# Optimization experiments

Measured on AMD Instinct MI355X. Metric: run time of the kernel, lower is better.

## Reference

```python
import jax, jax.numpy as jnp
import numpy as np

EMB = 8
HID = 64
B = 1000
T = 512
N = (B * T) // 5  # events per source; sources partition the (batch,time) grid

_KEYS = ["ccba", "cdtx", "cust", "dp", "remit"]
_NUMS = {"ccba": 8, "cdtx": 1, "cust": 1, "dp": 2, "remit": 1}
_CATS = {"ccba": 0, "cdtx": 2, "cust": 3, "dp": 8, "remit": 1}
_VOCAB = {"ccba": 0, "cdtx": 179, "cust": 37, "dp": 435, "remit": 5}


def setup_inputs() -> dict:
    ks = iter(jax.random.split(jax.random.key(0), 64))
    rng = np.random.default_rng(0)
    chunks = np.split(rng.permutation(B * T), 5)
    d = {}
    for k5, ch in zip(_KEYS, chunks):
        d[k5 + "_num"] = jax.random.normal(next(ks), (N, _NUMS[k5]), jnp.float32)
        if _CATS[k5] > 0:
            d[k5 + "_cat"] = jax.random.randint(next(ks), (N, _CATS[k5]), 0, _VOCAB[k5])
            d[k5 + "_tab"] = jax.random.normal(next(ks), (_VOCAB[k5], EMB), jnp.float32) * 0.1
        d[k5 + "_bi"] = jnp.asarray(ch // T, jnp.int32)
        d[k5 + "_ti"] = jnp.asarray(ch % T, jnp.int32)
        in_dim = _CATS[k5] * EMB + _NUMS[k5]
        d[k5 + "_W"] = jax.random.normal(next(ks), (in_dim, HID), jnp.float32) * np.float32(1.0 / np.sqrt(in_dim))
        d[k5 + "_b"] = jnp.zeros((HID,), jnp.float32)
    # LSTM: 2 layers x 2 directions, hidden 64, proj_size 1 -> layer1 input is 2
    for l, insz in [(0, HID), (1, 2)]:
        d[f"Wih{l}"] = jax.random.normal(next(ks), (2, 4 * HID, insz), jnp.float32) * 0.05
        d[f"Whh{l}"] = jax.random.normal(next(ks), (2, 4 * HID, 1), jnp.float32) * 0.05
        d[f"Whr{l}"] = jax.random.normal(next(ks), (2, 1, HID), jnp.float32) * 0.05
        d[f"bih{l}"] = jnp.zeros((2, 4 * HID), jnp.float32)
        d[f"bhh{l}"] = jnp.zeros((2, 4 * HID), jnp.float32)
    d["length"] = T
    d["batch_size"] = B
    return d


def _embed(num, cat, tab, W, b):
    # FeatureEmbedder: concat(categorical embeddings, numeric) -> Linear(hidden)
    x = num if cat is None else jnp.concatenate([tab[cat].reshape(cat.shape[0], -1), num], axis=-1)
    return x @ W + b


def _lstm_dir(x, Wih, Whh, Whr, bih, bhh, reverse):
    Bx = x.shape[0]
    H = Whr.shape[1]
    p = Whr.shape[0]
    bias = bih + bhh

    def step(carry, xt):
        h, c = carry  # h: [B,p] projected hidden, c: [B,H] cell
        g = xt @ Wih.T + h @ Whh.T + bias
        i, f, gg, o = jnp.split(g, 4, axis=-1)  # PyTorch gate order i,f,g,o
        c = jax.nn.sigmoid(f) * c + jax.nn.sigmoid(i) * jnp.tanh(gg)
        h = (jax.nn.sigmoid(o) * jnp.tanh(c)) @ Whr.T  # proj_size projection
        return (h, c), h

    init = (jnp.zeros((Bx, p), x.dtype), jnp.zeros((Bx, H), x.dtype))
    _, ys = jax.lax.scan(step, init, jnp.swapaxes(x, 0, 1), reverse=reverse)
    return jnp.swapaxes(ys, 0, 1)  # [B,T,p]


def _bilstm(x, Wih, Whh, Whr, bih, bhh):
    fwd = _lstm_dir(x, Wih[0], Whh[0], Whr[0], bih[0], bhh[0], False)
    bwd = _lstm_dir(x, Wih[1], Whh[1], Whr[1], bih[1], bhh[1], True)
    return jnp.concatenate([fwd, bwd], axis=-1)


def _forward(a):
    feat = jnp.zeros((a["batch_size"], a["length"], HID), jnp.float32)
    for k5 in _KEYS:
        v = _embed(a[k5 + "_num"], a.get(k5 + "_cat"), a.get(k5 + "_tab"), a[k5 + "_W"], a[k5 + "_b"])
        feat = feat.at[a[k5 + "_bi"], a[k5 + "_ti"]].set(v)  # scatter-assemble padded tensor
    h = _bilstm(feat, a["Wih0"], a["Whh0"], a["Whr0"], a["bih0"], a["bhh0"])
    h = _bilstm(h, a["Wih1"], a["Whh1"], a["Whr1"], a["bih1"], a["bhh1"])
    return h.mean(axis=2)  # [B,T]


def reference(ccba_num, ccba_bi, ccba_ti, ccba_W, ccba_b,
              cdtx_num, cdtx_cat, cdtx_tab, cdtx_bi, cdtx_ti, cdtx_W, cdtx_b,
              cust_num, cust_cat, cust_tab, cust_bi, cust_ti, cust_W, cust_b,
              dp_num, dp_cat, dp_tab, dp_bi, dp_ti, dp_W, dp_b,
              remit_num, remit_cat, remit_tab, remit_bi, remit_ti, remit_W, remit_b,
              Wih0, Whh0, Whr0, bih0, bhh0, Wih1, Whh1, Whr1, bih1, bhh1,
              length, batch_size):
    return _forward(dict(locals()))
```

## Files before the change

kernel.cpp:

```cpp
#include <hip/hip_runtime.h>
#include <cstdint>
#include <cstddef>

#define TLEN 512
#define BATCH 1000
#define NEVS 102400
#define HID 64
#define W0S 32

__device__ __forceinline__ float fast_rcp(float x) {
#if __has_builtin(__builtin_amdgcn_rcpf)
    return __builtin_amdgcn_rcpf(x);
#else
    return 1.0f / x;
#endif
}
__device__ __forceinline__ float sigm(float x) { return fast_rcp(1.0f + __expf(-x)); }
__device__ __forceinline__ float tanh_f(float x) { return fmaf(2.0f, sigm(2.0f * x), -1.0f); }

__device__ __forceinline__ float wave_sum_bcast(float x) {
#if __has_builtin(__builtin_amdgcn_update_dpp) && __has_builtin(__builtin_amdgcn_readlane)
    x += __int_as_float(__builtin_amdgcn_update_dpp(0, __float_as_int(x), 0x111, 0xf, 0xf, true));
    x += __int_as_float(__builtin_amdgcn_update_dpp(0, __float_as_int(x), 0x112, 0xf, 0xf, true));
    x += __int_as_float(__builtin_amdgcn_update_dpp(0, __float_as_int(x), 0x114, 0xf, 0xf, true));
    x += __int_as_float(__builtin_amdgcn_update_dpp(0, __float_as_int(x), 0x118, 0xf, 0xf, true));
    x += __int_as_float(__builtin_amdgcn_update_dpp(0, __float_as_int(x), 0x142, 0xa, 0xf, true));
    x += __int_as_float(__builtin_amdgcn_update_dpp(0, __float_as_int(x), 0x143, 0xc, 0xf, true));
    return __int_as_float(__builtin_amdgcn_readlane(__float_as_int(x), 63));
#else
#pragma unroll
    for (int off = 1; off < 64; off <<= 1) x += __shfl_xor(x, off, 64);
    return x;
#endif
}

__global__ __launch_bounds__(256) void map_build_kernel(
    const int* __restrict__ b0, const int* __restrict__ t0,
    const int* __restrict__ b1, const int* __restrict__ t1,
    const int* __restrict__ b2, const int* __restrict__ t2,
    const int* __restrict__ b3, const int* __restrict__ t3,
    const int* __restrict__ b4, const int* __restrict__ t4,
    int* __restrict__ map)
{
    const int src = blockIdx.y;
    const int* bi = src == 0 ? b0 : src == 1 ? b1 : src == 2 ? b2 : src == 3 ? b3 : b4;
    const int* ti = src == 0 ? t0 : src == 1 ? t1 : src == 2 ? t2 : src == 3 ? t3 : t4;
    const int e = blockIdx.x * 256 + threadIdx.x;
    map[bi[e] * TLEN + ti[e]] = (src << 20) | e;
}

__global__ __launch_bounds__(512) void compose_kernel(
    const float* __restrict__ W0, const float* __restrict__ B0,
    const float* __restrict__ W1, const float* __restrict__ B1,
    const float* __restrict__ W2, const float* __restrict__ B2,
    const float* __restrict__ W3, const float* __restrict__ B3,
    const float* __restrict__ W4, const float* __restrict__ B4,
    const float* __restrict__ Wih, const float* __restrict__ bih,
    const float* __restrict__ bhh, float* __restrict__ wp)
{
    const int col = threadIdx.x;
    const int row = blockIdx.x;
    const float* srcW; const float* srcB; int base, IND;
    if (row < 9)        { srcW = W0; srcB = B0; base = 0;   IND = 8;  }
    else if (row < 27)  { srcW = W1; srcB = B1; base = 9;   IND = 17; }
    else if (row < 53)  { srcW = W2; srcB = B2; base = 27;  IND = 25; }
    else if (row < 120) { srcW = W3; srcB = B3; base = 53;  IND = 66; }
    else                { srcW = W4; srcB = B4; base = 120; IND = 9;  }
    const int j = row - base;
    const float* xrow = (j < IND) ? (srcW + (size_t)j * 64) : srcB;
    const float* wr = Wih + (size_t)col * 64;
    float acc = 0.0f;
#pragma unroll
    for (int h2 = 0; h2 < 64; ++h2) acc = fmaf(xrow[h2], wr[h2], acc);
    if (j == IND) acc += bih[col] + bhh[col];
    wp[(size_t)row * 512 + col] = acc;
}

__global__ __launch_bounds__(256) void fused0_kernel(
    const float* __restrict__ ccba_num,
    const float* __restrict__ cdtx_num, const int* __restrict__ cdtx_cat, const float* __restrict__ cdtx_tab,
    const float* __restrict__ cust_num, const int* __restrict__ cust_cat, const float* __restrict__ cust_tab,
    const float* __restrict__ dp_num,   const int* __restrict__ dp_cat,   const float* __restrict__ dp_tab,
    const float* __restrict__ remit_num, const int* __restrict__ remit_cat, const float* __restrict__ remit_tab,
    const float* __restrict__ wp, const int* __restrict__ map,
    const float* __restrict__ Whh, const float* __restrict__ Whr,
    float* __restrict__ h0)
{
    const int tid = threadIdx.x;
    const int b = blockIdx.x >> 1, dir = blockIdx.x & 1;
    const int col = dir * 256 + tid;

    float w_c0[9], w_c1[18], w_c2[26], w_c3[67], w_c4[10];
#pragma unroll
    for (int j = 0; j < 9;  ++j) w_c0[j] = wp[(size_t)(0   + j) * 512 + col];
#pragma unroll
    for (int j = 0; j < 18; ++j) w_c1[j] = wp[(size_t)(9   + j) * 512 + col];
#pragma unroll
    for (int j = 0; j < 26; ++j) w_c2[j] = wp[(size_t)(27  + j) * 512 + col];
#pragma unroll
    for (int j = 0; j < 67; ++j) w_c3[j] = wp[(size_t)(53  + j) * 512 + col];
#pragma unroll
    for (int j = 0; j < 10; ++j) w_c4[j] = wp[(size_t)(120 + j) * 512 + col];

    __shared__ float window[W0S * 256];
    __shared__ float xbuf[W0S][68];
    __shared__ int   mcls[W0S];

    const int lane = tid & 63;
    float whh4[4] = {0, 0, 0, 0};
    float whr = 0.0f, h = 0.0f, c = 0.0f;
    if (tid < 64) {
#pragma unroll
        for (int k = 0; k < 4; ++k) whh4[k] = Whh[dir * 256 + k * 64 + lane];
        whr = Whr[dir * HID + lane];
    }
    float* h0p = h0 + (size_t)b * TLEN * 2 + dir;

    auto dot_evt = [&](int mc, const float* xb) -> float {
        const int src = mc >> 20;
        float a0 = 0.0f, a1 = 0.0f, bias = 0.0f;
        switch (src) {
        case 0:
#pragma unroll
            for (int j = 0; j < 8; j += 2) { a0 = fmaf(xb[j], w_c0[j], a0); a1 = fmaf(xb[j + 1], w_c0[j + 1], a1); }
            bias = w_c0[8]; break;
        case 1:
#pragma unroll
            for (int j = 0; j < 16; j += 2) { a0 = fmaf(xb[j], w_c1[j], a0); a1 = fmaf(xb[j + 1], w_c1[j + 1], a1); }
            a0 = fmaf(xb[16], w_c1[16], a0);
            bias = w_c1[17]; break;
        case 2:
#pragma unroll
            for (int j = 0; j < 24; j += 2) { a0 = fmaf(xb[j], w_c2[j], a0); a1 = fmaf(xb[j + 1], w_c2[j + 1], a1); }
            a0 = fmaf(xb[24], w_c2[24], a0);
            bias = w_c2[25]; break;
        case 3:
#pragma unroll
            for (int j = 0; j < 66; j += 2) { a0 = fmaf(xb[j], w_c3[j], a0); a1 = fmaf(xb[j + 1], w_c3[j + 1], a1); }
            bias = w_c3[66]; break;
        default:
#pragma unroll
            for (int j = 0; j < 8; j += 2) { a0 = fmaf(xb[j], w_c4[j], a0); a1 = fmaf(xb[j + 1], w_c4[j + 1], a1); }
            a0 = fmaf(xb[8], w_c4[8], a0);
            bias = w_c4[9]; break;
        }
        return bias + a0 + a1;
    };

    for (int s0 = 0; s0 < TLEN; s0 += W0S) {
        {
            const int sl = tid >> 3, q = tid & 7;
            const int s = s0 + sl;
            const int t = dir ? (TLEN - 1 - s) : s;
            const int mc = map[b * TLEN + t];
            if (q == 0) mcls[sl] = mc;
            const int src = mc >> 20, e = mc & 0xFFFFF;
            switch (src) {
            case 0:
                for (int v = q; v < 8; v += 8) xbuf[sl][v] = ccba_num[(size_t)e * 8 + v];
                break;
            case 1:
                for (int v = q; v < 17; v += 8) {
                    float x = (v < 16) ? cdtx_tab[(size_t)cdtx_cat[e * 2 + (v >> 3)] * 8 + (v & 7)]
                                       : cdtx_num[e];
                    xbuf[sl][v] = x;
                }
                break;
            case 2:
                for (int v = q; v < 25; v += 8) {
                    float x = (v < 24) ? cust_tab[(size_t)cust_cat[e * 3 + (v >> 3)] * 8 + (v & 7)]
                                       : cust_num[e];
                    xbuf[sl][v] = x;
                }
                break;
            case 3:
                for (int v = q; v < 66; v += 8) {
                    float x = (v < 64) ? dp_tab[(size_t)dp_cat[e * 8 + (v >> 3)] * 8 + (v & 7)]
                                       : dp_num[(size_t)e * 2 + (v - 64)];
                    xbuf[sl][v] = x;
                }
                break;
            default:
                for (int v = q; v < 9; v += 8) {
                    float x = (v < 8) ? remit_tab[(size_t)remit_cat[e] * 8 + v]
                                      : remit_num[e];
                    xbuf[sl][v] = x;
                }
                break;
            }
        }
        __syncthreads();

        for (int sl = 0; sl < W0S; sl += 2) {
            const float accA = dot_evt(mcls[sl], xbuf[sl]);
            const float accB = dot_evt(mcls[sl + 1], xbuf[sl + 1]);
            window[sl * 256 + tid] = accA;
            window[(sl + 1) * 256 + tid] = accB;
        }
        __syncthreads();

        if (tid < 64) {
            float G[4], N[4];
#pragma unroll
            for (int k = 0; k < 4; ++k) G[k] = window[k * 64 + lane];
            for (int sl = 0; sl < W0S; ++sl) {
                const int slp = (sl + 1 < W0S) ? (sl + 1) : sl;
#pragma unroll
                for (int k = 0; k < 4; ++k) N[k] = window[slp * 256 + k * 64 + lane];
                const float gi = fmaf(whh4[0], h, G[0]);
                const float gf = fmaf(whh4[1], h, G[1]);
                const float gg = fmaf(whh4[2], h, G[2]);
                const float go = fmaf(whh4[3], h, G[3]);
                c = sigm(gf) * c + sigm(gi) * tanh_f(gg);
                h = wave_sum_bcast(sigm(go) * tanh_f(c) * whr);
                const int s = s0 + sl;
                const int t = dir ? (TLEN - 1 - s) : s;
                if (lane == 0) h0p[(size_t)t * 2] = h;
#pragma unroll
                for (int k = 0; k < 4; ++k) G[k] = N[k];
            }
        }
        __syncthreads();
    }
}

__global__ __launch_bounds__(256) void lstm1_kernel(
    const float* __restrict__ h0, const float* __restrict__ Wih,
    const float* __restrict__ Whh, const float* __restrict__ Whr,
    const float* __restrict__ bih, const float* __restrict__ bhh,
    float* __restrict__ h1)
{
    int w = threadIdx.x >> 6, lane = threadIdx.x & 63;
    int p = blockIdx.x * 4 + w;
    int b = p >> 1, dir = p & 1;

    float wi0[4], wi1[4], whh[4], bias[4];
#pragma unroll
    for (int k = 0; k < 4; ++k) {
        int r = k * 64 + lane;
        wi0[k] = Wih[(size_t)(dir * 256 + r) * 2 + 0];
        wi1[k] = Wih[(size_t)(dir * 256 + r) * 2 + 1];
        whh[k] = Whh[dir * 256 + r];
        bias[k] = bih[dir * 256 + r] + bhh[dir * 256 + r];
    }
    float whr = Whr[dir * HID + lane];
    float h = 0.0f, c = 0.0f;
    const float* hb = h0 + (size_t)b * TLEN * 2;

    auto xat = [&](int t) -> float2 {
        int tc = t < TLEN ? t : TLEN - 1;
        int tt = dir ? (TLEN - 1 - tc) : tc;
        return *(const float2*)(hb + (size_t)tt * 2);
    };

    float2 xA = xat(0), xB = xat(1);
    for (int t = 0; t < TLEN; t += 2) {
        float2 xC = xat(t + 2), xD = xat(t + 3);
        {
            float g[4];
#pragma unroll
            for (int k = 0; k < 4; ++k)
                g[k] = fmaf(whh[k], h, fmaf(wi1[k], xA.y, fmaf(wi0[k], xA.x, bias[k])));
            c = sigm(g[1]) * c + sigm(g[0]) * tanh_f(g[2]);
            h = wave_sum_bcast(sigm(g[3]) * tanh_f(c) * whr);
            int tt = dir ? (TLEN - 1 - t) : t;
            if (lane == 0) h1[((size_t)b * TLEN + tt) * 2 + dir] = h;
        }
        {
            float g[4];
#pragma unroll
            for (int k = 0; k < 4; ++k)
                g[k] = fmaf(whh[k], h, fmaf(wi1[k], xB.y, fmaf(wi0[k], xB.x, bias[k])));
            c = sigm(g[1]) * c + sigm(g[0]) * tanh_f(g[2]);
            h = wave_sum_bcast(sigm(g[3]) * tanh_f(c) * whr);
            int tt = dir ? (TLEN - 2 - t) : (t + 1);
            if (lane == 0) h1[((size_t)b * TLEN + tt) * 2 + dir] = h;
        }
        xA = xC; xB = xD;
    }
}

__global__ __launch_bounds__(256) void mean_kernel(
    const float2* __restrict__ h1, float* __restrict__ out)
{
    int i = blockIdx.x * 256 + threadIdx.x;
    if (i < BATCH * TLEN) {
        float2 v = h1[i];
        out[i] = 0.5f * (v.x + v.y);
    }
}

extern "C" void kernel_launch(void* const* d_in, const int* in_sizes, int n_in,
                              void* d_out, int out_size, void* d_ws, size_t ws_size,
                              hipStream_t stream)
{
    const float* ccba_num = (const float*)d_in[0];
    const int*   ccba_bi  = (const int*)d_in[1];
    const int*   ccba_ti  = (const int*)d_in[2];
    const float* ccba_W   = (const float*)d_in[3];
    const float* ccba_b   = (const float*)d_in[4];
    const float* cdtx_num = (const float*)d_in[5];
    const int*   cdtx_cat = (const int*)d_in[6];
    const float* cdtx_tab = (const float*)d_in[7];
    const int*   cdtx_bi  = (const int*)d_in[8];
    const int*   cdtx_ti  = (const int*)d_in[9];
    const float* cdtx_W   = (const float*)d_in[10];
    const float* cdtx_b   = (const float*)d_in[11];
    const float* cust_num = (const float*)d_in[12];
    const int*   cust_cat = (const int*)d_in[13];
    const float* cust_tab = (const float*)d_in[14];
    const int*   cust_bi  = (const int*)d_in[15];
    const int*   cust_ti  = (const int*)d_in[16];
    const float* cust_W   = (const float*)d_in[17];
    const float* cust_b   = (const float*)d_in[18];
    const float* dp_num   = (const float*)d_in[19];
    const int*   dp_cat   = (const int*)d_in[20];
    const float* dp_tab   = (const float*)d_in[21];
    const int*   dp_bi    = (const int*)d_in[22];
    const int*   dp_ti    = (const int*)d_in[23];
    const float* dp_W     = (const float*)d_in[24];
    const float* dp_b     = (const float*)d_in[25];
    const float* remit_num = (const float*)d_in[26];
    const int*   remit_cat = (const int*)d_in[27];
    const float* remit_tab = (const float*)d_in[28];
    const int*   remit_bi  = (const int*)d_in[29];
    const int*   remit_ti  = (const int*)d_in[30];
    const float* remit_W   = (const float*)d_in[31];
    const float* remit_b   = (const float*)d_in[32];
    const float* Wih0 = (const float*)d_in[33];
    const float* Whh0 = (const float*)d_in[34];
    const float* Whr0 = (const float*)d_in[35];
    const float* bih0 = (const float*)d_in[36];
    const float* bhh0 = (const float*)d_in[37];
    const float* Wih1 = (const float*)d_in[38];
    const float* Whh1 = (const float*)d_in[39];
    const float* Whr1 = (const float*)d_in[40];
    const float* bih1 = (const float*)d_in[41];
    const float* bhh1 = (const float*)d_in[42];

    float* out = (float*)d_out;

    char* ws = (char*)d_ws;
    float* wp  = (float*)ws;
    int*   map = (int*)  (ws + 266240ull);
    float* h0  = (float*)(ws + 266240ull + 2048000ull);
    float* h1  = (float*)(ws + 266240ull + 2048000ull + 4096000ull);

    compose_kernel<<<130, 512, 0, stream>>>(
        ccba_W, ccba_b, cdtx_W, cdtx_b, cust_W, cust_b,
        dp_W, dp_b, remit_W, remit_b, Wih0, bih0, bhh0, wp);

    map_build_kernel<<<dim3(NEVS / 256, 5), 256, 0, stream>>>(
        ccba_bi, ccba_ti, cdtx_bi, cdtx_ti, cust_bi, cust_ti,
        dp_bi, dp_ti, remit_bi, remit_ti, map);

    fused0_kernel<<<2 * BATCH, 256, 0, stream>>>(
        ccba_num,
        cdtx_num, cdtx_cat, cdtx_tab,
        cust_num, cust_cat, cust_tab,
        dp_num, dp_cat, dp_tab,
        remit_num, remit_cat, remit_tab,
        wp, map, Whh0, Whr0, h0);

    lstm1_kernel<<<500, 256, 0, stream>>>(h0, Wih1, Whh1, Whr1, bih1, bhh1, h1);
    mean_kernel<<<(BATCH * TLEN + 255) / 256, 256, 0, stream>>>((const float2*)h1, out);
}
```

Measured before the change: 1.623 ms.

## Split layer-0 input dots across 512 threads, double-buffer gathers, interleave LSTM1 directions

After: 1.478 ms. 9.0% less time.

```diff
diff --git a/kernel.cpp b/kernel.cpp
--- a/kernel.cpp
+++ b/kernel.cpp
@@ -6,7 +6,8 @@
 #define BATCH 1000
 #define NEVS 102400
 #define HID 64
-#define W0S 32
+#define W0S 16
+#define NP (TLEN / W0S)
 
 __device__ __forceinline__ float fast_rcp(float x) {
 #if __has_builtin(__builtin_amdgcn_rcpf)
@@ -31,6 +32,34 @@
 #pragma unroll
     for (int off = 1; off < 64; off <<= 1) x += __shfl_xor(x, off, 64);
     return x;
+#endif
+}
+
+__device__ __forceinline__ void wave_sum2(float& a, float& b) {
+#if __has_builtin(__builtin_amdgcn_update_dpp) && __has_builtin(__builtin_amdgcn_readlane)
+    int ta, tb;
+    ta = __builtin_amdgcn_update_dpp(0, __float_as_int(a), 0x111, 0xf, 0xf, true);
+    tb = __builtin_amdgcn_update_dpp(0, __float_as_int(b), 0x111, 0xf, 0xf, true);
+    a += __int_as_float(ta); b += __int_as_float(tb);
+    ta = __builtin_amdgcn_update_dpp(0, __float_as_int(a), 0x112, 0xf, 0xf, true);
+    tb = __builtin_amdgcn_update_dpp(0, __float_as_int(b), 0x112, 0xf, 0xf, true);
+    a += __int_as_float(ta); b += __int_as_float(tb);
+    ta = __builtin_amdgcn_update_dpp(0, __float_as_int(a), 0x114, 0xf, 0xf, true);
+    tb = __builtin_amdgcn_update_dpp(0, __float_as_int(b), 0x114, 0xf, 0xf, true);
+    a += __int_as_float(ta); b += __int_as_float(tb);
+    ta = __builtin_amdgcn_update_dpp(0, __float_as_int(a), 0x118, 0xf, 0xf, true);
+    tb = __builtin_amdgcn_update_dpp(0, __float_as_int(b), 0x118, 0xf, 0xf, true);
+    a += __int_as_float(ta); b += __int_as_float(tb);
+    ta = __builtin_amdgcn_update_dpp(0, __float_as_int(a), 0x142, 0xa, 0xf, true);
+    tb = __builtin_amdgcn_update_dpp(0, __float_as_int(b), 0x142, 0xa, 0xf, true);
+    a += __int_as_float(ta); b += __int_as_float(tb);
+    ta = __builtin_amdgcn_update_dpp(0, __float_as_int(a), 0x143, 0xc, 0xf, true);
+    tb = __builtin_amdgcn_update_dpp(0, __float_as_int(b), 0x143, 0xc, 0xf, true);
+    a += __int_as_float(ta); b += __int_as_float(tb);
+    a = __int_as_float(__builtin_amdgcn_readlane(__float_as_int(a), 63));
+    b = __int_as_float(__builtin_amdgcn_readlane(__float_as_int(b), 63));
+#else
+    a = wave_sum_bcast(a); b = wave_sum_bcast(b);
 #endif
 }
 
@@ -76,7 +105,181 @@
     wp[(size_t)row * 512 + col] = acc;
 }
 
-__global__ __launch_bounds__(256) void fused0_kernel(
+template<bool HI>
+__device__ __forceinline__ void fused_path(
+    const float* __restrict__ wp, const int* __restrict__ map,
+    const float* __restrict__ ccba_num,
+    const float* __restrict__ cdtx_num, const int* __restrict__ cdtx_cat, const float* __restrict__ cdtx_tab,
+    const float* __restrict__ cust_num, const int* __restrict__ cust_cat, const float* __restrict__ cust_tab,
+    const float* __restrict__ dp_num,   const int* __restrict__ dp_cat,   const float* __restrict__ dp_tab,
+    const float* __restrict__ remit_num, const int* __restrict__ remit_cat, const float* __restrict__ remit_tab,
+    const float* __restrict__ Whh, const float* __restrict__ Whr,
+    float* __restrict__ h0, int b, int dir, int tid,
+    float (&winP)[2][W0S][256], float (&xbuf)[2][W0S][68], int (&mcls)[2][W0S])
+{
+    constexpr int C0 = HI ? 3 : 5,  O0 = HI ? 5 : 0;
+    constexpr int C1 = HI ? 8 : 9,  O1 = HI ? 9 : 0;
+    constexpr int C2 = HI ? 12 : 13, O2 = HI ? 13 : 0;
+    constexpr int C3 = HI ? 32 : 34, O3 = HI ? 34 : 0;
+    constexpr int C4 = HI ? 4 : 5,  O4 = HI ? 5 : 0;
+
+    const int pcol = tid & 255;
+    const int col = dir * 256 + pcol;
+
+    float w0[C0], w1[C1], w2[C2], w3[C3], w4[C4];
+#pragma unroll
+    for (int j = 0; j < C0; ++j) w0[j] = wp[(size_t)(0 + O0 + j) * 512 + col];
+#pragma unroll
+    for (int j = 0; j < C1; ++j) w1[j] = wp[(size_t)(9 + O1 + j) * 512 + col];
+#pragma unroll
+    for (int j = 0; j < C2; ++j) w2[j] = wp[(size_t)(27 + O2 + j) * 512 + col];
+#pragma unroll
+    for (int j = 0; j < C3; ++j) w3[j] = wp[(size_t)(53 + O3 + j) * 512 + col];
+#pragma unroll
+    for (int j = 0; j < C4; ++j) w4[j] = wp[(size_t)(120 + O4 + j) * 512 + col];
+    float bias0 = 0, bias1 = 0, bias2 = 0, bias3 = 0, bias4 = 0;
+    if (HI) {
+        bias0 = wp[(size_t)8 * 512 + col];
+        bias1 = wp[(size_t)26 * 512 + col];
+        bias2 = wp[(size_t)52 * 512 + col];
+        bias3 = wp[(size_t)119 * 512 + col];
+        bias4 = wp[(size_t)129 * 512 + col];
+    }
+
+    const int lane = tid & 63;
+    float whh4[4] = {0, 0, 0, 0};
+    float whr = 0.0f, h = 0.0f, c = 0.0f;
+    if (!HI && tid < 64) {
+#pragma unroll
+        for (int k = 0; k < 4; ++k) whh4[k] = Whh[dir * 256 + k * 64 + lane];
+        whr = Whr[dir * HID + lane];
+    }
+    float* h0p = h0 + (size_t)b * TLEN * 2 + dir;
+
+    auto dot_evt = [&](int mc, const float* xb) -> float {
+        const int src = mc >> 20;
+        float a0 = 0.f, a1 = 0.f, bb = 0.f;
+        switch (src) {
+        case 0:
+#pragma unroll
+            for (int j = 0; j < C0; ++j) {
+                if (j & 1) a1 = fmaf(xb[O0 + j], w0[j], a1); else a0 = fmaf(xb[O0 + j], w0[j], a0);
+            }
+            bb = bias0; break;
+        case 1:
+#pragma unroll
+            for (int j = 0; j < C1; ++j) {
+                if (j & 1) a1 = fmaf(xb[O1 + j], w1[j], a1); else a0 = fmaf(xb[O1 + j], w1[j], a0);
+            }
+            bb = bias1; break;
+        case 2:
+#pragma unroll
+            for (int j = 0; j < C2; ++j) {
+                if (j & 1) a1 = fmaf(xb[O2 + j], w2[j], a1); else a0 = fmaf(xb[O2 + j], w2[j], a0);
+            }
+            bb = bias2; break;
+        case 3:
+#pragma unroll
+            for (int j = 0; j < C3; ++j) {
+                if (j & 1) a1 = fmaf(xb[O3 + j], w3[j], a1); else a0 = fmaf(xb[O3 + j], w3[j], a0);
+            }
+            bb = bias3; break;
+        default:
+#pragma unroll
+            for (int j = 0; j < C4; ++j) {
+                if (j & 1) a1 = fmaf(xb[O4 + j], w4[j], a1); else a0 = fmaf(xb[O4 + j], w4[j], a0);
+            }
+            bb = bias4; break;
+        }
+        return HI ? (bb + a0 + a1) : (a0 + a1);
+    };
+
+    auto gather_phase = [&](int P, int slot) {
+        const int ev = tid >> 5, v = tid & 31;
+        const int s = P * W0S + ev;
+        const int t = dir ? (TLEN - 1 - s) : s;
+        const int mc = map[b * TLEN + t];
+        if (v == 0) mcls[slot][ev] = mc;
+        const int src = mc >> 20, e = mc & 0xFFFFF;
+        switch (src) {
+        case 0:
+            if (v < 8) xbuf[slot][ev][v] = ccba_num[(size_t)e * 8 + v];
+            break;
+        case 1:
+            if (v < 17) xbuf[slot][ev][v] = (v < 16)
+                ? cdtx_tab[(size_t)cdtx_cat[e * 2 + (v >> 3)] * 8 + (v & 7)] : cdtx_num[e];
+            break;
+        case 2:
+            if (v < 25) xbuf[slot][ev][v] = (v < 24)
+                ? cust_tab[(size_t)cust_cat[e * 3 + (v >> 3)] * 8 + (v & 7)] : cust_num[e];
+            break;
+        case 3:
+#pragma unroll
+            for (int vv = v; vv < 66; vv += 32)
+                xbuf[slot][ev][vv] = (vv < 64)
+                    ? dp_tab[(size_t)dp_cat[e * 8 + (vv >> 3)] * 8 + (vv & 7)]
+                    : dp_num[(size_t)e * 2 + (vv - 64)];
+            break;
+        default:
+            if (v < 9) xbuf[slot][ev][v] = (v < 8)
+                ? remit_tab[(size_t)remit_cat[e] * 8 + v] : remit_num[e];
+            break;
+        }
+    };
+
+    auto dots_phase = [&](int slot) {
+#pragma unroll 1
+        for (int sl = 0; sl < W0S; sl += 2) {
+            const int mc0 = mcls[slot][sl];
+            const int mc1 = mcls[slot][sl + 1];
+            const float a = dot_evt(mc0, xbuf[slot][sl]);
+            const float bq = dot_evt(mc1, xbuf[slot][sl + 1]);
+            winP[HI ? 1 : 0][sl][pcol] = a;
+            winP[HI ? 1 : 0][sl + 1][pcol] = bq;
+        }
+    };
+
+    gather_phase(0, 0);
+    __syncthreads();
+
+    for (int p = 0; p < NP; ++p) {
+        if (p + 1 < NP) gather_phase(p + 1, (p + 1) & 1);
+        dots_phase(p & 1);
+        __syncthreads();
+
+        if (!HI && tid < 64) {
+            float G0[4], G1[4];
+#pragma unroll
+            for (int k = 0; k < 4; ++k) {
+                G0[k] = winP[0][0][k * 64 + lane];
+                G1[k] = winP[1][0][k * 64 + lane];
+            }
+            for (int sl = 0; sl < W0S; ++sl) {
+                const int sn = (sl + 1 < W0S) ? sl + 1 : sl;
+                float N0[4], N1[4];
+#pragma unroll
+                for (int k = 0; k < 4; ++k) {
+                    N0[k] = winP[0][sn][k * 64 + lane];
+                    N1[k] = winP[1][sn][k * 64 + lane];
+                }
+                const float gi = fmaf(whh4[0], h, G0[0] + G1[0]);
+                const float gf = fmaf(whh4[1], h, G0[1] + G1[1]);
+                const float gg = fmaf(whh4[2], h, G0[2] + G1[2]);
+                const float go = fmaf(whh4[3], h, G0[3] + G1[3]);
+                c = sigm(gf) * c + sigm(gi) * tanh_f(gg);
+                h = wave_sum_bcast(sigm(go) * tanh_f(c) * whr);
+                const int s = p * W0S + sl;
+                const int t = dir ? (TLEN - 1 - s) : s;
+                if (lane == 0) h0p[(size_t)t * 2] = h;
+#pragma unroll
+                for (int k = 0; k < 4; ++k) { G0[k] = N0[k]; G1[k] = N1[k]; }
+            }
+        }
+        __syncthreads();
+    }
+}
+
+__global__ __launch_bounds__(512, 4) void fused0_kernel(
     const float* __restrict__ ccba_num,
     const float* __restrict__ cdtx_num, const int* __restrict__ cdtx_cat, const float* __restrict__ cdtx_tab,
     const float* __restrict__ cust_num, const int* __restrict__ cust_cat, const float* __restrict__ cust_tab,
@@ -86,142 +289,21 @@
     const float* __restrict__ Whh, const float* __restrict__ Whr,
     float* __restrict__ h0)
 {
+    __shared__ float winP[2][W0S][256];
+    __shared__ float xbuf[2][W0S][68];
+    __shared__ int   mcls[2][W0S];
     const int tid = threadIdx.x;
     const int b = blockIdx.x >> 1, dir = blockIdx.x & 1;
-    const int col = dir * 256 + tid;
-
-    float w_c0[9], w_c1[18], w_c2[26], w_c3[67], w_c4[10];
-#pragma unroll
-    for (int j = 0; j < 9;  ++j) w_c0[j] = wp[(size_t)(0   + j) * 512 + col];
-#pragma unroll
-    for (int j = 0; j < 18; ++j) w_c1[j] = wp[(size_t)(9   + j) * 512 + col];
-#pragma unroll
-    for (int j = 0; j < 26; ++j) w_c2[j] = wp[(size_t)(27  + j) * 512 + col];
-#pragma unroll
-    for (int j = 0; j < 67; ++j) w_c3[j] = wp[(size_t)(53  + j) * 512 + col];
-#pragma unroll
-    for (int j = 0; j < 10; ++j) w_c4[j] = wp[(size_t)(120 + j) * 512 + col];
-
-    __shared__ float window[W0S * 256];
-    __shared__ float xbuf[W0S][68];
-    __shared__ int   mcls[W0S];
-
-    const int lane = tid & 63;
-    float whh4[4] = {0, 0, 0, 0};
-    float whr = 0.0f, h = 0.0f, c = 0.0f;
-    if (tid < 64) {
-#pragma unroll
-        for (int k = 0; k < 4; ++k) whh4[k] = Whh[dir * 256 + k * 64 + lane];
-        whr = Whr[dir * HID + lane];
-    }
-    float* h0p = h0 + (size_t)b * TLEN * 2 + dir;
-
-    auto dot_evt = [&](int mc, const float* xb) -> float {
-        const int src = mc >> 20;
-        float a0 = 0.0f, a1 = 0.0f, bias = 0.0f;
-        switch (src) {
-        case 0:
-#pragma unroll
-            for (int j = 0; j < 8; j += 2) { a0 = fmaf(xb[j], w_c0[j], a0); a1 = fmaf(xb[j + 1], w_c0[j + 1], a1); }
-            bias = w_c0[8]; break;
-        case 1:
-#pragma unroll
-            for (int j = 0; j < 16; j += 2) { a0 = fmaf(xb[j], w_c1[j], a0); a1 = fmaf(xb[j + 1], w_c1[j + 1], a1); }
-            a0 = fmaf(xb[16], w_c1[16], a0);
-            bias = w_c1[17]; break;
-        case 2:
-#pragma unroll
-            for (int j = 0; j < 24; j += 2) { a0 = fmaf(xb[j], w_c2[j], a0); a1 = fmaf(xb[j + 1], w_c2[j + 1], a1); }
-            a0 = fmaf(xb[24], w_c2[24], a0);
-            bias = w_c2[25]; break;
-        case 3:
-#pragma unroll
-            for (int j = 0; j < 66; j += 2) { a0 = fmaf(xb[j], w_c3[j], a0); a1 = fmaf(xb[j + 1], w_c3[j + 1], a1); }
-            bias = w_c3[66]; break;
-        default:
-#pragma unroll
-            for (int j = 0; j < 8; j += 2) { a0 = fmaf(xb[j], w_c4[j], a0); a1 = fmaf(xb[j + 1], w_c4[j + 1], a1); }
-            a0 = fmaf(xb[8], w_c4[8], a0);
-            bias = w_c4[9]; break;
-        }
-        return bias + a0 + a1;
-    };
-
-    for (int s0 = 0; s0 < TLEN; s0 += W0S) {
-        {
-            const int sl = tid >> 3, q = tid & 7;
-            const int s = s0 + sl;
-            const int t = dir ? (TLEN - 1 - s) : s;
-            const int mc = map[b * TLEN + t];
-            if (q == 0) mcls[sl] = mc;
-            const int src = mc >> 20, e = mc & 0xFFFFF;
-            switch (src) {
-            case 0:
-                for (int v = q; v < 8; v += 8) xbuf[sl][v] = ccba_num[(size_t)e * 8 + v];
-                break;
-            case 1:
-                for (int v = q; v < 17; v += 8) {
-                    float x = (v < 16) ? cdtx_tab[(size_t)cdtx_cat[e * 2 + (v >> 3)] * 8 + (v & 7)]
-                                       : cdtx_num[e];
-                    xbuf[sl][v] = x;
-                }
-                break;
-            case 2:
-                for (int v = q; v < 25; v += 8) {
-                    float x = (v < 24) ? cust_tab[(size_t)cust_cat[e * 3 + (v >> 3)] * 8 + (v & 7)]
-                                       : cust_num[e];
-                    xbuf[sl][v] = x;
-                }
-                break;
-            case 3:
-                for (int v = q; v < 66; v += 8) {
-                    float x = (v < 64) ? dp_tab[(size_t)dp_cat[e * 8 + (v >> 3)] * 8 + (v & 7)]
-                                       : dp_num[(size_t)e * 2 + (v - 64)];
-                    xbuf[sl][v] = x;
-                }
-                break;
-            default:
-                for (int v = q; v < 9; v += 8) {
-                    float x = (v < 8) ? remit_tab[(size_t)remit_cat[e] * 8 + v]
-                                      : remit_num[e];
-                    xbuf[sl][v] = x;
-                }
-                break;
-            }
-        }
-        __syncthreads();
-
-        for (int sl = 0; sl < W0S; sl += 2) {
-            const float accA = dot_evt(mcls[sl], xbuf[sl]);
-            const float accB = dot_evt(mcls[sl + 1], xbuf[sl + 1]);
-            window[sl * 256 + tid] = accA;
-            window[(sl + 1) * 256 + tid] = accB;
-        }
-        __syncthreads();
-
-        if (tid < 64) {
-            float G[4], N[4];
-#pragma unroll
-            for (int k = 0; k < 4; ++k) G[k] = window[k * 64 + lane];
-            for (int sl = 0; sl < W0S; ++sl) {
-                const int slp = (sl + 1 < W0S) ? (sl + 1) : sl;
-#pragma unroll
-                for (int k = 0; k < 4; ++k) N[k] = window[slp * 256 + k * 64 + lane];
-                const float gi = fmaf(whh4[0], h, G[0]);
-                const float gf = fmaf(whh4[1], h, G[1]);
-                const float gg = fmaf(whh4[2], h, G[2]);
-                const float go = fmaf(whh4[3], h, G[3]);
-                c = sigm(gf) * c + sigm(gi) * tanh_f(gg);
-                h = wave_sum_bcast(sigm(go) * tanh_f(c) * whr);
-                const int s = s0 + sl;
-                const int t = dir ? (TLEN - 1 - s) : s;
-                if (lane == 0) h0p[(size_t)t * 2] = h;
-#pragma unroll
-                for (int k = 0; k < 4; ++k) G[k] = N[k];
-            }
-        }
-        __syncthreads();
-    }
+    if (tid < 256)
+        fused_path<false>(wp, map, ccba_num,
+            cdtx_num, cdtx_cat, cdtx_tab, cust_num, cust_cat, cust_tab,
+            dp_num, dp_cat, dp_tab, remit_num, remit_cat, remit_tab,
+            Whh, Whr, h0, b, dir, tid, winP, xbuf, mcls);
+    else
+        fused_path<true>(wp, map, ccba_num,
+            cdtx_num, cdtx_cat, cdtx_tab, cust_num, cust_cat, cust_tab,
+            dp_num, dp_cat, dp_tab, remit_num, remit_cat, remit_tab,
+            Whh, Whr, h0, b, dir, tid, winP, xbuf, mcls);
 }
 
 __global__ __launch_bounds__(256) void lstm1_kernel(
@@ -230,53 +312,48 @@
     const float* __restrict__ bih, const float* __restrict__ bhh,
     float* __restrict__ h1)
 {
-    int w = threadIdx.x >> 6, lane = threadIdx.x & 63;
-    int p = blockIdx.x * 4 + w;
-    int b = p >> 1, dir = p & 1;
-
-    float wi0[4], wi1[4], whh[4], bias[4];
-#pragma unroll
-    for (int k = 0; k < 4; ++k) {
-        int r = k * 64 + lane;
-        wi0[k] = Wih[(size_t)(dir * 256 + r) * 2 + 0];
-        wi1[k] = Wih[(size_t)(dir * 256 + r) * 2 + 1];
-        whh[k] = Whh[dir * 256 + r];
-        bias[k] = bih[dir * 256 + r] + bhh[dir * 256 + r];
-    }
-    float whr = Whr[dir * HID + lane];
-    float h = 0.0f, c = 0.0f;
+    const int w = threadIdx.x >> 6, lane = threadIdx.x & 63;
+    const int b = blockIdx.x * 4 + w;
+
+    float wi0[2][4], wi1[2][4], whh[2][4], bias[2][4], whr[2];
+#pragma unroll
+    for (int d = 0; d < 2; ++d) {
+#pragma unroll
+        for (int k = 0; k < 4; ++k) {
+            const int r = d * 256 + k * 64 + lane;
+            wi0[d][k] = Wih[(size_t)r * 2 + 0];
+            wi1[d][k] = Wih[(size_t)r * 2 + 1];
+            whh[d][k] = Whh[r];
+            bias[d][k] = bih[r] + bhh[r];
+        }
+        whr[d] = Whr[d * HID + lane];
+    }
+    float hA = 0, cA = 0, hB = 0, cB = 0;
     const float* hb = h0 + (size_t)b * TLEN * 2;
 
-    auto xat = [&](int t) -> float2 {
-        int tc = t < TLEN ? t : TLEN - 1;
-        int tt = dir ? (TLEN - 1 - tc) : tc;
-        return *(const float2*)(hb + (size_t)tt * 2);
-    };
-
-    float2 xA = xat(0), xB = xat(1);
-    for (int t = 0; t < TLEN; t += 2) {
-        float2 xC = xat(t + 2), xD = xat(t + 3);
-        {
-            float g[4];
-#pragma unroll
-            for (int k = 0; k < 4; ++k)
-                g[k] = fmaf(whh[k], h, fmaf(wi1[k], xA.y, fmaf(wi0[k], xA.x, bias[k])));
-            c = sigm(g[1]) * c + sigm(g[0]) * tanh_f(g[2]);
-            h = wave_sum_bcast(sigm(g[3]) * tanh_f(c) * whr);
-            int tt = dir ? (TLEN - 1 - t) : t;
-            if (lane == 0) h1[((size_t)b * TLEN + tt) * 2 + dir] = h;
-        }
-        {
-            float g[4];
-#pragma unroll
-            for (int k = 0; k < 4; ++k)
-                g[k] = fmaf(whh[k], h, fmaf(wi1[k], xB.y, fmaf(wi0[k], xB.x, bias[k])));
-            c = sigm(g[1]) * c + sigm(g[0]) * tanh_f(g[2]);
-            h = wave_sum_bcast(sigm(g[3]) * tanh_f(c) * whr);
-            int tt = dir ? (TLEN - 2 - t) : (t + 1);
-            if (lane == 0) h1[((size_t)b * TLEN + tt) * 2 + dir] = h;
-        }
-        xA = xC; xB = xD;
+    float2 xA = *(const float2*)(hb);
+    float2 xB = *(const float2*)(hb + (size_t)(TLEN - 1) * 2);
+    for (int t = 0; t < TLEN; ++t) {
+        const int tn = (t + 1 < TLEN) ? t + 1 : t;
+        const float2 xAn = *(const float2*)(hb + (size_t)tn * 2);
+        const float2 xBn = *(const float2*)(hb + (size_t)(TLEN - 1 - tn) * 2);
+        float gA[4], gB[4];
+#pragma unroll
+        for (int k = 0; k < 4; ++k) {
+            gA[k] = fmaf(whh[0][k], hA, fmaf(wi1[0][k], xA.y, fmaf(wi0[0][k], xA.x, bias[0][k])));
+            gB[k] = fmaf(whh[1][k], hB, fmaf(wi1[1][k], xB.y, fmaf(wi0[1][k], xB.x, bias[1][k])));
+        }
+        cA = sigm(gA[1]) * cA + sigm(gA[0]) * tanh_f(gA[2]);
+        cB = sigm(gB[1]) * cB + sigm(gB[0]) * tanh_f(gB[2]);
+        float pA = sigm(gA[3]) * tanh_f(cA) * whr[0];
+        float pB = sigm(gB[3]) * tanh_f(cB) * whr[1];
+        wave_sum2(pA, pB);
+        hA = pA; hB = pB;
+        if (lane == 0) {
+            h1[((size_t)b * TLEN + t) * 2 + 0] = hA;
+            h1[((size_t)b * TLEN + (TLEN - 1 - t)) * 2 + 1] = hB;
+        }
+        xA = xAn; xB = xBn;
     }
 }
 
@@ -354,7 +431,7 @@
         ccba_bi, ccba_ti, cdtx_bi, cdtx_ti, cust_bi, cust_ti,
         dp_bi, dp_ti, remit_bi, remit_ti, map);
 
-    fused0_kernel<<<2 * BATCH, 256, 0, stream>>>(
+    fused0_kernel<<<2 * BATCH, 512, 0, stream>>>(
         ccba_num,
         cdtx_num, cdtx_cat, cdtx_tab,
         cust_num, cust_cat, cust_tab,
@@ -362,6 +439,6 @@
         remit_num, remit_cat, remit_tab,
         wp, map, Whh0, Whr0, h0);
 
-    lstm1_kernel<<<500, 256, 0, stream>>>(h0, Wih1, Whh1, Whr1, bih1, bhh1, h1);
+    lstm1_kernel<<<250, 256, 0, stream>>>(h0, Wih1, Whh1, Whr1, bih1, bhh1, h1);
     mean_kernel<<<(BATCH * TLEN + 255) / 256, 256, 0, stream>>>((const float2*)h1, out);
 }
```
